# Kernel tuning notes

Measured on AMD Instinct MI355X. Metric: run time of the kernel, lower is better.

## Reference

```python
import jax, jax.numpy as jnp
import numpy as np

B, N, F_IN, M, U = 2, 2048, 128, 8, 64


def setup_inputs() -> dict:
    key = jax.random.key(0)
    k1, k2, k3, k4 = jax.random.split(key, 4)
    seq_data = jax.random.normal(k1, (B, N, F_IN), dtype=jnp.float32)
    # weighted multi-layer digraph adjacency (B, N_to, N_from, M)
    graph = jax.random.uniform(k2, (B, N, N, M), dtype=jnp.float32)
    e_weight = jax.random.normal(k3, (F_IN, U), dtype=jnp.float32) * (1.0 / np.sqrt(F_IN))
    v_weight = jax.random.normal(k4, (F_IN, M, U), dtype=jnp.float32) * (1.0 / np.sqrt(F_IN))
    return {"seq_data": seq_data, "graph": graph, "e_weight": e_weight, "v_weight": v_weight}


def reference(seq_data, graph, e_weight, v_weight):
    # beta = seq_data @ e_weight : (B, N, U)
    beta = jnp.einsum('bnf,fu->bnu', seq_data, e_weight)
    # _batch_dot(graph, beta, axes=(2,1)) -> einsum 'bijm,bju->bimu'
    out = jnp.einsum('bijm,bju->bimu', graph, beta)
    # node self-loop term: reshape-free einsum of v_weight (F_in, M, U)
    alpha = jnp.einsum('bnf,fmu->bnmu', seq_data, v_weight)
    return jax.nn.sigmoid(out + alpha)  # (B, N, M, U)
```

## Files before the change

kernel.cpp:

```cpp
#include <hip/hip_runtime.h>
#include <cmath>

#define N_ 2048
#define F_ 128
#define M_ 8
#define U_ 64

typedef _Float16 f16;
typedef _Float16 f16x2 __attribute__((ext_vector_type(2)));
typedef _Float16 f16x8 __attribute__((ext_vector_type(8)));
typedef float f32x4 __attribute__((ext_vector_type(4)));

#define BK 32
#define RS 40
#define NCH (N_ / BK)

__global__ __launch_bounds__(256) void k_beta(const float* __restrict__ seq,
                                              const float* __restrict__ ew,
                                              f16* __restrict__ bh,
                                              f16* __restrict__ bl) {
  __shared__ float st[16 * 132];
  const int t    = threadIdx.x;
  const int lane = t & 63;
  const int wv   = t >> 6;
  const int row0 = blockIdx.x * 16;
#pragma unroll
  for (int k = 0; k < 2; ++k) {
    int id = t + k * 256;
    int r = id >> 5, f4 = id & 31;
    float4 v = *(const float4*)(seq + (size_t)(row0 + r) * F_ + f4 * 4);
    *(float4*)&st[r * 132 + f4 * 4] = v;
  }
  __syncthreads();
  const int r0 = wv * 4;
  float acc[4] = {0.f, 0.f, 0.f, 0.f};
#pragma unroll 8
  for (int f = 0; f < F_; ++f) {
    float e = ew[f * U_ + lane];
#pragma unroll
    for (int r = 0; r < 4; ++r)
      acc[r] = fmaf(st[(r0 + r) * 132 + f], e, acc[r]);
  }
#pragma unroll
  for (int r = 0; r < 4; ++r) {
    int row = row0 + r0 + r;
    int b = row >> 11, n = row & (N_ - 1);
    float v = acc[r];
    f16 h = (f16)v;
    f16 l = (f16)(v - (float)h);
    size_t idx = ((size_t)(b * U_ + lane)) * N_ + n;
    bh[idx] = h;
    bl[idx] = l;
  }
}

__global__ __launch_bounds__(256, 2) void k_alpha(const float* __restrict__ seq,
                                                  const float* __restrict__ vw,
                                                  float* __restrict__ out) {
  __shared__ float ss[8 * 128];
  const int t    = threadIdx.x;
  const int q    = t & 15;
  const int g    = t >> 4;
  const int r    = g & 7;
  const int mh   = g >> 3;
  const int row0 = blockIdx.x * 8;
  {
    float4 v = *(const float4*)(seq + (size_t)row0 * F_ + t * 4);
    *(float4*)&ss[t * 4] = v;
  }
  __syncthreads();
  float acc[4][4] = {};
  const float* wbase = vw + mh * 4 * 64 + q * 4;
#pragma unroll 4
  for (int f = 0; f < F_; ++f) {
    float s = ss[r * F_ + f];
    const float* wf = wbase + (size_t)f * 512;
#pragma unroll
    for (int mm = 0; mm < 4; ++mm) {
      float4 wv = *(const float4*)(wf + mm * 64);
      acc[mm][0] = fmaf(s, wv.x, acc[mm][0]);
      acc[mm][1] = fmaf(s, wv.y, acc[mm][1]);
      acc[mm][2] = fmaf(s, wv.z, acc[mm][2]);
      acc[mm][3] = fmaf(s, wv.w, acc[mm][3]);
    }
  }
  float* o = out + (size_t)(row0 + r) * 512 + mh * 4 * 64 + q * 4;
#pragma unroll
  for (int mm = 0; mm < 4; ++mm) {
    float4 res;
    res.x = acc[mm][0]; res.y = acc[mm][1];
    res.z = acc[mm][2]; res.w = acc[mm][3];
    *(float4*)(o + mm * 64) = res;
  }
}

__global__ __launch_bounds__(256, 2) void k_main(const float* __restrict__ graph,
                                                 const f16* __restrict__ betah,
                                                 const f16* __restrict__ betal,
                                                 float* __restrict__ out) {
  __shared__ f16 Ah[2][64 * RS];
  __shared__ f16 Al[2][64 * RS];
  __shared__ f16 Bh[2][64 * RS];
  __shared__ f16 Bl[2][64 * RS];

  const int t    = threadIdx.x;
  const int w    = t >> 6;
  const int lane = t & 63;
  const int l15  = lane & 15;
  const int quad = lane >> 4;

  const int bx = blockIdx.x;
  const int b  = bx >> 8;
  const int rb = bx & 255;

  const int iA = t >> 5;
  const int r5 = t & 31;
  const int jp = r5 >> 1;
  const int mh = r5 & 1;
  const int uB = t >> 2;
  const int pB = t & 3;

  const float* gA = graph + ((size_t)(b * N_ + rb * 8 + iA)) * (N_ * M_) + mh * 4;
  const f16* bhp = betah + ((size_t)(b * U_ + uB)) * N_ + pB * 8;
  const f16* blp = betal + ((size_t)(b * U_ + uB)) * N_ + pB * 8;

  f32x4 acc[4] = {f32x4{0.f, 0.f, 0.f, 0.f}, f32x4{0.f, 0.f, 0.f, 0.f},
                  f32x4{0.f, 0.f, 0.f, 0.f}, f32x4{0.f, 0.f, 0.f, 0.f}};

  float4 ra0_0, ra1_0; uint4 rbh_0, rbl_0;
  float4 ra0_1, ra1_1; uint4 rbh_1, rbl_1;

#define LOADC(c, S)                                                       \
  do {                                                                    \
    const float* g_ = gA + (size_t)((c) * BK + jp * 2) * M_;              \
    ra0_##S = *(const float4*)g_;                                         \
    ra1_##S = *(const float4*)(g_ + M_);                                  \
    rbh_##S = *(const uint4*)(bhp + (c) * BK);                            \
    rbl_##S = *(const uint4*)(blp + (c) * BK);                            \
  } while (0)

#define WRITEC(buf, S)                                                    \
  do {                                                                    \
    float g0s[4] = {ra0_##S.x, ra0_##S.y, ra0_##S.z, ra0_##S.w};          \
    float g1s[4] = {ra1_##S.x, ra1_##S.y, ra1_##S.z, ra1_##S.w};          \
    _Pragma("unroll") for (int mw = 0; mw < 4; ++mw) {                    \
      float g0 = g0s[mw], g1 = g1s[mw];                                   \
      f16 h0 = (f16)g0, h1 = (f16)g1;                                     \
      f16 l0 = (f16)(g0 - (float)h0), l1 = (f16)(g1 - (float)h1);         \
      int r_ = iA * 8 + mh * 4 + mw;                                      \
      f16x2 hv; hv[0] = h0; hv[1] = h1;                                   \
      f16x2 lv; lv[0] = l0; lv[1] = l1;                                   \
      *(f16x2*)&Ah[buf][r_ * RS + jp * 2] = hv;                           \
      *(f16x2*)&Al[buf][r_ * RS + jp * 2] = lv;                           \
    }                                                                     \
    *(uint4*)&Bh[buf][uB * RS + pB * 8] = rbh_##S;                        \
    *(uint4*)&Bl[buf][uB * RS + pB * 8] = rbl_##S;                        \
  } while (0)

#define COMPUTE(buf)                                                      \
  do {                                                                    \
    const int ab_ = (w * 16 + l15) * RS + quad * 8;                       \
    f16x8 ah = *(const f16x8*)&Ah[buf][ab_];                              \
    f16x8 al = *(const f16x8*)&Al[buf][ab_];                              \
    _Pragma("unroll") for (int ut = 0; ut < 4; ++ut) {                    \
      const int bb_ = (ut * 16 + l15) * RS + quad * 8;                    \
      f16x8 bhf = *(const f16x8*)&Bh[buf][bb_];                           \
      f16x8 blf = *(const f16x8*)&Bl[buf][bb_];                           \
      acc[ut] = __builtin_amdgcn_mfma_f32_16x16x32_f16(ah, bhf, acc[ut], 0, 0, 0); \
      acc[ut] = __builtin_amdgcn_mfma_f32_16x16x32_f16(al, bhf, acc[ut], 0, 0, 0); \
      acc[ut] = __builtin_amdgcn_mfma_f32_16x16x32_f16(ah, blf, acc[ut], 0, 0, 0); \
    }                                                                     \
  } while (0)

#define BAR()                                                             \
  do {                                                                    \
    asm volatile("s_waitcnt lgkmcnt(0)" ::: "memory");                    \
    __builtin_amdgcn_s_barrier();                                         \
    asm volatile("" ::: "memory");                                        \
  } while (0)

  LOADC(0, 0);
  WRITEC(0, 0);
  LOADC(1, 1);
  BAR();

  for (int cc = 0; cc < NCH - 4; cc += 2) {
    COMPUTE(0);
    LOADC(cc + 2, 0);
    WRITEC(1, 1);
    BAR();
    COMPUTE(1);
    LOADC(cc + 3, 1);
    WRITEC(0, 0);
    BAR();
  }

  COMPUTE(0);
  LOADC(NCH - 2, 0);
  WRITEC(1, 1);
  BAR();
  COMPUTE(1);
  LOADC(NCH - 1, 1);
  WRITEC(0, 0);
  BAR();
  COMPUTE(0);
  WRITEC(1, 1);
  BAR();
  COMPUTE(1);

  const int rowbase = rb * 64 + w * 16 + quad * 4;
#pragma unroll
  for (int ut = 0; ut < 4; ++ut) {
    const int u = ut * 16 + l15;
#pragma unroll
    for (int reg = 0; reg < 4; ++reg) {
      size_t idx = ((size_t)(b * 16384 + rowbase + reg)) * U_ + u;
      float x = acc[ut][reg] + out[idx];
      out[idx] = 1.0f / (1.0f + __expf(-x));
    }
  }
#undef LOADC
#undef WRITEC
#undef COMPUTE
#undef BAR
}

extern "C" void kernel_launch(void* const* d_in, const int* in_sizes, int n_in,
                              void* d_out, int out_size, void* d_ws, size_t ws_size,
                              hipStream_t stream) {
  const float* seq   = (const float*)d_in[0];
  const float* graph = (const float*)d_in[1];
  const float* ew    = (const float*)d_in[2];
  const float* vw    = (const float*)d_in[3];
  float* out = (float*)d_out;

  f16* betah = (f16*)d_ws;
  f16* betal = betah + (size_t)2 * U_ * N_;

  hipLaunchKernelGGL(k_beta,  dim3(256), dim3(256), 0, stream, seq, ew, betah, betal);
  hipLaunchKernelGGL(k_alpha, dim3(512), dim3(256), 0, stream, seq, vw, out);
  hipLaunchKernelGGL(k_main,  dim3(512), dim3(256), 0, stream, graph, betah, betal, out);
}
```

Baseline: 409.5 us.

## Merge beta and alpha prologue kernels; use 2x2 wave tiling in main GEMM

The separate beta and alpha precompute kernels become one launch that branches on block index, which removes a kernel launch and its gap. In the main kernel each wave now computes a 32x32 output tile (2x2 MFMA tiles) instead of 16x64. This cuts the LDS fragment loads per MFMA, since B fragments are reused across two M tiles. The main kernel is dominated by streaming the 268MB graph, so the gain from either change may be small.

```diff
diff --git a/kernel.cpp b/kernel.cpp
--- a/kernel.cpp
+++ b/kernel.cpp
@@ -15,82 +15,81 @@
 #define RS 40
 #define NCH (N_ / BK)
 
-__global__ __launch_bounds__(256) void k_beta(const float* __restrict__ seq,
-                                              const float* __restrict__ ew,
-                                              f16* __restrict__ bh,
-                                              f16* __restrict__ bl) {
-  __shared__ float st[16 * 132];
-  const int t    = threadIdx.x;
-  const int lane = t & 63;
-  const int wv   = t >> 6;
-  const int row0 = blockIdx.x * 16;
-#pragma unroll
-  for (int k = 0; k < 2; ++k) {
-    int id = t + k * 256;
-    int r = id >> 5, f4 = id & 31;
-    float4 v = *(const float4*)(seq + (size_t)(row0 + r) * F_ + f4 * 4);
-    *(float4*)&st[r * 132 + f4 * 4] = v;
-  }
-  __syncthreads();
-  const int r0 = wv * 4;
-  float acc[4] = {0.f, 0.f, 0.f, 0.f};
+__global__ __launch_bounds__(256) void k_pre(const float* __restrict__ seq,
+                                             const float* __restrict__ ew,
+                                             const float* __restrict__ vw,
+                                             f16* __restrict__ bh,
+                                             f16* __restrict__ bl,
+                                             float* __restrict__ out) {
+  __shared__ float smem[16 * 132];
+  const int t = threadIdx.x;
+
+  if (blockIdx.x < 512) {
+    const int q    = t & 15;
+    const int g    = t >> 4;
+    const int r    = g & 7;
+    const int mh   = g >> 3;
+    const int row0 = blockIdx.x * 8;
+    {
+      float4 v = *(const float4*)(seq + (size_t)row0 * F_ + t * 4);
+      *(float4*)&smem[t * 4] = v;
+    }
+    __syncthreads();
+    float acc[4][4] = {};
+    const float* wbase = vw + mh * 4 * 64 + q * 4;
+#pragma unroll 4
+    for (int f = 0; f < F_; ++f) {
+      float s = smem[r * F_ + f];
+      const float* wf = wbase + (size_t)f * 512;
+#pragma unroll
+      for (int mm = 0; mm < 4; ++mm) {
+        float4 wv = *(const float4*)(wf + mm * 64);
+        acc[mm][0] = fmaf(s, wv.x, acc[mm][0]);
+        acc[mm][1] = fmaf(s, wv.y, acc[mm][1]);
+        acc[mm][2] = fmaf(s, wv.z, acc[mm][2]);
+        acc[mm][3] = fmaf(s, wv.w, acc[mm][3]);
+      }
+    }
+    float* o = out + (size_t)(row0 + r) * 512 + mh * 4 * 64 + q * 4;
+#pragma unroll
+    for (int mm = 0; mm < 4; ++mm) {
+      float4 res;
+      res.x = acc[mm][0]; res.y = acc[mm][1];
+      res.z = acc[mm][2]; res.w = acc[mm][3];
+      *(float4*)(o + mm * 64) = res;
+    }
+  } else {
+    const int lane = t & 63;
+    const int wv   = t >> 6;
+    const int row0 = (blockIdx.x - 512) * 16;
+#pragma unroll
+    for (int k = 0; k < 2; ++k) {
+      int id = t + k * 256;
+      int r = id >> 5, f4 = id & 31;
+      float4 v = *(const float4*)(seq + (size_t)(row0 + r) * F_ + f4 * 4);
+      *(float4*)&smem[r * 132 + f4 * 4] = v;
+    }
+    __syncthreads();
+    const int r0 = wv * 4;
+    float acc[4] = {0.f, 0.f, 0.f, 0.f};
 #pragma unroll 8
-  for (int f = 0; f < F_; ++f) {
-    float e = ew[f * U_ + lane];
-#pragma unroll
-    for (int r = 0; r < 4; ++r)
-      acc[r] = fmaf(st[(r0 + r) * 132 + f], e, acc[r]);
-  }
-#pragma unroll
-  for (int r = 0; r < 4; ++r) {
-    int row = row0 + r0 + r;
-    int b = row >> 11, n = row & (N_ - 1);
-    float v = acc[r];
-    f16 h = (f16)v;
-    f16 l = (f16)(v - (float)h);
-    size_t idx = ((size_t)(b * U_ + lane)) * N_ + n;
-    bh[idx] = h;
-    bl[idx] = l;
-  }
-}
-
-__global__ __launch_bounds__(256, 2) void k_alpha(const float* __restrict__ seq,
-                                                  const float* __restrict__ vw,
-                                                  float* __restrict__ out) {
-  __shared__ float ss[8 * 128];
-  const int t    = threadIdx.x;
-  const int q    = t & 15;
-  const int g    = t >> 4;
-  const int r    = g & 7;
-  const int mh   = g >> 3;
-  const int row0 = blockIdx.x * 8;
-  {
-    float4 v = *(const float4*)(seq + (size_t)row0 * F_ + t * 4);
-    *(float4*)&ss[t * 4] = v;
-  }
-  __syncthreads();
-  float acc[4][4] = {};
-  const float* wbase = vw + mh * 4 * 64 + q * 4;
-#pragma unroll 4
-  for (int f = 0; f < F_; ++f) {
-    float s = ss[r * F_ + f];
-    const float* wf = wbase + (size_t)f * 512;
-#pragma unroll
-    for (int mm = 0; mm < 4; ++mm) {
-      float4 wv = *(const float4*)(wf + mm * 64);
-      acc[mm][0] = fmaf(s, wv.x, acc[mm][0]);
-      acc[mm][1] = fmaf(s, wv.y, acc[mm][1]);
-      acc[mm][2] = fmaf(s, wv.z, acc[mm][2]);
-      acc[mm][3] = fmaf(s, wv.w, acc[mm][3]);
-    }
-  }
-  float* o = out + (size_t)(row0 + r) * 512 + mh * 4 * 64 + q * 4;
-#pragma unroll
-  for (int mm = 0; mm < 4; ++mm) {
-    float4 res;
-    res.x = acc[mm][0]; res.y = acc[mm][1];
-    res.z = acc[mm][2]; res.w = acc[mm][3];
-    *(float4*)(o + mm * 64) = res;
+    for (int f = 0; f < F_; ++f) {
+      float e = ew[f * U_ + lane];
+#pragma unroll
+      for (int r = 0; r < 4; ++r)
+        acc[r] = fmaf(smem[(r0 + r) * 132 + f], e, acc[r]);
+    }
+#pragma unroll
+    for (int r = 0; r < 4; ++r) {
+      int row = row0 + r0 + r;
+      int b = row >> 11, n = row & (N_ - 1);
+      float v = acc[r];
+      f16 h = (f16)v;
+      f16 l = (f16)(v - (float)h);
+      size_t idx = ((size_t)(b * U_ + lane)) * N_ + n;
+      bh[idx] = h;
+      bl[idx] = l;
+    }
   }
 }
 
@@ -108,6 +107,8 @@
   const int lane = t & 63;
   const int l15  = lane & 15;
   const int quad = lane >> 4;
+  const int wr   = w >> 1;
+  const int wc   = w & 1;
 
   const int bx = blockIdx.x;
   const int b  = bx >> 8;
@@ -124,8 +125,8 @@
   const f16* bhp = betah + ((size_t)(b * U_ + uB)) * N_ + pB * 8;
   const f16* blp = betal + ((size_t)(b * U_ + uB)) * N_ + pB * 8;
 
-  f32x4 acc[4] = {f32x4{0.f, 0.f, 0.f, 0.f}, f32x4{0.f, 0.f, 0.f, 0.f},
-                  f32x4{0.f, 0.f, 0.f, 0.f}, f32x4{0.f, 0.f, 0.f, 0.f}};
+  f32x4 acc[2][2] = {{f32x4{0.f, 0.f, 0.f, 0.f}, f32x4{0.f, 0.f, 0.f, 0.f}},
+                     {f32x4{0.f, 0.f, 0.f, 0.f}, f32x4{0.f, 0.f, 0.f, 0.f}}};
 
   float4 ra0_0, ra1_0; uint4 rbh_0, rbl_0;
   float4 ra0_1, ra1_1; uint4 rbh_1, rbl_1;
@@ -159,16 +160,21 @@
 
 #define COMPUTE(buf)                                                      \
   do {                                                                    \
-    const int ab_ = (w * 16 + l15) * RS + quad * 8;                       \
-    f16x8 ah = *(const f16x8*)&Ah[buf][ab_];                              \
-    f16x8 al = *(const f16x8*)&Al[buf][ab_];                              \
-    _Pragma("unroll") for (int ut = 0; ut < 4; ++ut) {                    \
-      const int bb_ = (ut * 16 + l15) * RS + quad * 8;                    \
-      f16x8 bhf = *(const f16x8*)&Bh[buf][bb_];                           \
-      f16x8 blf = *(const f16x8*)&Bl[buf][bb_];                           \
-      acc[ut] = __builtin_amdgcn_mfma_f32_16x16x32_f16(ah, bhf, acc[ut], 0, 0, 0); \
-      acc[ut] = __builtin_amdgcn_mfma_f32_16x16x32_f16(al, bhf, acc[ut], 0, 0, 0); \
-      acc[ut] = __builtin_amdgcn_mfma_f32_16x16x32_f16(ah, blf, acc[ut], 0, 0, 0); \
+    f16x8 bhf[2], blf[2];                                                 \
+    _Pragma("unroll") for (int nt = 0; nt < 2; ++nt) {                    \
+      const int bb_ = (wc * 32 + nt * 16 + l15) * RS + quad * 8;          \
+      bhf[nt] = *(const f16x8*)&Bh[buf][bb_];                             \
+      blf[nt] = *(const f16x8*)&Bl[buf][bb_];                             \
+    }                                                                     \
+    _Pragma("unroll") for (int mt = 0; mt < 2; ++mt) {                    \
+      const int ab_ = (wr * 32 + mt * 16 + l15) * RS + quad * 8;          \
+      f16x8 ah = *(const f16x8*)&Ah[buf][ab_];                            \
+      f16x8 al = *(const f16x8*)&Al[buf][ab_];                            \
+      _Pragma("unroll") for (int nt = 0; nt < 2; ++nt) {                  \
+        acc[mt][nt] = __builtin_amdgcn_mfma_f32_16x16x32_f16(ah, bhf[nt], acc[mt][nt], 0, 0, 0); \
+        acc[mt][nt] = __builtin_amdgcn_mfma_f32_16x16x32_f16(al, bhf[nt], acc[mt][nt], 0, 0, 0); \
+        acc[mt][nt] = __builtin_amdgcn_mfma_f32_16x16x32_f16(ah, blf[nt], acc[mt][nt], 0, 0, 0); \
+      }                                                                   \
     }                                                                     \
   } while (0)
 
@@ -208,15 +214,18 @@
   BAR();
   COMPUTE(1);
 
-  const int rowbase = rb * 64 + w * 16 + quad * 4;
-#pragma unroll
-  for (int ut = 0; ut < 4; ++ut) {
-    const int u = ut * 16 + l15;
-#pragma unroll
-    for (int reg = 0; reg < 4; ++reg) {
-      size_t idx = ((size_t)(b * 16384 + rowbase + reg)) * U_ + u;
-      float x = acc[ut][reg] + out[idx];
-      out[idx] = 1.0f / (1.0f + __expf(-x));
+  const int rowbase = rb * 64 + wr * 32 + quad * 4;
+#pragma unroll
+  for (int mt = 0; mt < 2; ++mt) {
+#pragma unroll
+    for (int nt = 0; nt < 2; ++nt) {
+      const int u = wc * 32 + nt * 16 + l15;
+#pragma unroll
+      for (int reg = 0; reg < 4; ++reg) {
+        size_t idx = ((size_t)(b * 16384 + rowbase + mt * 16 + reg)) * U_ + u;
+        float x = acc[mt][nt][reg] + out[idx];
+        out[idx] = 1.0f / (1.0f + __expf(-x));
+      }
     }
   }
 #undef LOADC
@@ -237,7 +246,6 @@
   f16* betah = (f16*)d_ws;
   f16* betal = betah + (size_t)2 * U_ * N_;
 
-  hipLaunchKernelGGL(k_beta,  dim3(256), dim3(256), 0, stream, seq, ew, betah, betal);
-  hipLaunchKernelGGL(k_alpha, dim3(512), dim3(256), 0, stream, seq, vw, out);
-  hipLaunchKernelGGL(k_main,  dim3(512), dim3(256), 0, stream, graph, betah, betal, out);
+  hipLaunchKernelGGL(k_pre,  dim3(768), dim3(256), 0, stream, seq, ew, vw, betah, betal, out);
+  hipLaunchKernelGGL(k_main, dim3(512), dim3(256), 0, stream, graph, betah, betal, out);
 }
```

Result: faster. 401.3 us (-2.0%).
